# Performance work log

Hardware: AMD Instinct MI355X
Metric: run time of the kernel (lower is better)

The kernel has to match this reference:

```python
import jax, jax.numpy as jnp
import numpy as np

N = 100000
E = 1600000
H = 8
C = 16
DIM = 128
EDGE_DIM = 32


def setup_inputs() -> dict:
    key = jax.random.key(0)
    ks = jax.random.split(key, 7)
    s = 1.0 / np.sqrt(DIM)
    return {
        "x": jax.random.normal(ks[0], (N, DIM), dtype=jnp.float32),
        "edge_index": jax.random.randint(ks[1], (2, E), 0, N, dtype=jnp.int32),
        "edge_attr": jax.random.normal(ks[2], (E, EDGE_DIM), dtype=jnp.float32),
        "Wq": jax.random.normal(ks[3], (H * C, DIM), dtype=jnp.float32) * s,
        "Wk": jax.random.normal(ks[4], (H * C, DIM), dtype=jnp.float32) * s,
        "Wv": jax.random.normal(ks[5], (H * C, DIM), dtype=jnp.float32) * s,
        "We": jax.random.normal(ks[6], (H, EDGE_DIM), dtype=jnp.float32) * (1.0 / np.sqrt(EDGE_DIM)),
    }


def reference(x, edge_index, edge_attr, Wq, Wk, Wv, We):
    # Node projections: [N, H, C]
    q = (x @ Wq.T).reshape(N, H, C)
    k = (x @ Wk.T).reshape(N, H, C)
    v = (x @ Wv.T).reshape(N, H, C)

    src, dst = edge_index[0], edge_index[1]

    # Per-edge attention logits with edge bias: [E, H]
    edge_bias = edge_attr @ We.T
    scores = jnp.einsum("ehc,ehc->eh", q[dst], k[src]) / np.sqrt(C) + edge_bias

    # Numerically-stable segment softmax over destination groups
    seg_max = jax.ops.segment_max(scores, dst, num_segments=N)  # [N, H]
    ex = jnp.exp(scores - seg_max[dst])
    denom = jax.ops.segment_sum(ex, dst, num_segments=N)  # [N, H]
    alpha = ex / denom[dst]  # [E, H]

    # Scale gathered values and scatter-add to destinations
    msgs = v[src] * alpha[:, :, None]  # [E, H, C]
    out = jax.ops.segment_sum(msgs, dst, num_segments=N)  # [N, H, C]
    return out.reshape(N, H * C)
```

## Files before the change

### kernel.cpp

```cpp
#include <hip/hip_runtime.h>


typedef unsigned int uint32;

__device__ inline unsigned short f2bf(float f) {
    uint32 u = __float_as_uint(f);
    uint32 r = u + 0x7fffu + ((u >> 16) & 1u);
    return (unsigned short)(r >> 16);
}

template <int CTRL>
__device__ inline float dpp_mov(float v) {
    return __int_as_float(__builtin_amdgcn_update_dpp(
        0, __float_as_int(v), CTRL, 0xF, 0xF, true));
}

__global__ __launch_bounds__(256) void qkv_count_kernel(
    const float* __restrict__ x,
    const float* __restrict__ Wq,
    const float* __restrict__ Wk,
    const float* __restrict__ Wv,
    const float* __restrict__ We,
    const float* __restrict__ edge_attr,
    const int* __restrict__ edge_index,
    float* __restrict__ q,
    unsigned short* __restrict__ kbf,
    unsigned short* __restrict__ vbf,
    float* __restrict__ ebias,
    int* __restrict__ counts,
    int N, int E)
{
    if (blockIdx.y == 6) {
        int idx = blockIdx.x * 256 + threadIdx.x;
        if (idx * 4 + 3 < E) {
            int4 d4 = ((const int4*)(edge_index + E))[idx];
            atomicAdd(&counts[d4.x], 1);
            atomicAdd(&counts[d4.y], 1);
            atomicAdd(&counts[d4.z], 1);
            atomicAdd(&counts[d4.w], 1);
        } else {
            for (int e = idx * 4; e < E; ++e)
                atomicAdd(&counts[edge_index[(size_t)E + e]], 1);
        }
        return;
    }

    if (blockIdx.y == 7) {
        const int t  = threadIdx.x;
        const int h  = t & 7;
        const int er = t >> 3;
        float4 wreg[8];
#pragma unroll
        for (int i = 0; i < 8; ++i)
            wreg[i] = *(const float4*)(We + h * 32 + i * 4);
        const int e0 = blockIdx.x * 1024;
        for (int it = 0; it < 32; ++it) {
            int e = e0 + it * 32 + er;
            if (e < E) {
                const float* ea = edge_attr + (size_t)e * 32;
                float s = 0.f;
#pragma unroll
                for (int i = 0; i < 8; ++i) {
                    float4 a = *(const float4*)(ea + i * 4);
                    float4 w = wreg[i];
                    s += a.x * w.x + a.y * w.y + a.z * w.z + a.w * w.w;
                }
                ebias[(size_t)e * 8 + h] = s;
            }
        }
        return;
    }

    const int nb = blockIdx.x * 64;
    const int cb = blockIdx.y * 64;
    const float* __restrict__ W = (cb < 128) ? Wq : (cb < 256) ? Wk : Wv;
    const int wrow0 = cb & 127;

    __shared__ float As[16][68];
    __shared__ float Bs[16][68];

    const int tid = threadIdx.x;
    const int tx = tid & 15;
    const int ty = tid >> 4;

    float acc[4][4] = {};

    const int lrow = tid >> 2;
    const int lk   = (tid & 3) * 4;
    const int n_load = nb + lrow;

    for (int k0 = 0; k0 < 128; k0 += 16) {
        float4 a = make_float4(0.f, 0.f, 0.f, 0.f);
        if (n_load < N)
            a = *(const float4*)(x + (size_t)n_load * 128 + k0 + lk);
        float4 b = *(const float4*)(W + (size_t)(wrow0 + lrow) * 128 + k0 + lk);
        As[lk + 0][lrow] = a.x; As[lk + 1][lrow] = a.y;
        As[lk + 2][lrow] = a.z; As[lk + 3][lrow] = a.w;
        Bs[lk + 0][lrow] = b.x; Bs[lk + 1][lrow] = b.y;
        Bs[lk + 2][lrow] = b.z; Bs[lk + 3][lrow] = b.w;
        __syncthreads();
#pragma unroll
        for (int kk = 0; kk < 16; ++kk) {
            float4 av = *(const float4*)&As[kk][ty * 4];
            float4 bv = *(const float4*)&Bs[kk][tx * 4];
            float avr[4] = {av.x, av.y, av.z, av.w};
            float bvr[4] = {bv.x, bv.y, bv.z, bv.w};
#pragma unroll
            for (int i = 0; i < 4; ++i)
#pragma unroll
                for (int j = 0; j < 4; ++j)
                    acc[i][j] = fmaf(avr[i], bvr[j], acc[i][j]);
        }
        __syncthreads();
    }

#pragma unroll
    for (int i = 0; i < 4; ++i) {
        int n = nb + ty * 4 + i;
        if (n >= N) continue;
        if (cb < 128) {
            float4 o = make_float4(acc[i][0], acc[i][1], acc[i][2], acc[i][3]);
            *(float4*)(q + (size_t)n * 128 + wrow0 + tx * 4) = o;
        } else {
            unsigned short* kv = (cb < 256) ? kbf : vbf;
            ushort4 o;
            o.x = f2bf(acc[i][0]); o.y = f2bf(acc[i][1]);
            o.z = f2bf(acc[i][2]); o.w = f2bf(acc[i][3]);
            *(ushort4*)(kv + (size_t)n * 128 + wrow0 + tx * 4) = o;
        }
    }
}

__global__ __launch_bounds__(256) void scan_pass1(
    const int* __restrict__ counts, int* __restrict__ blocksums, int N)
{
    __shared__ int red[256];
    int base = blockIdx.x * 512;
    int t = threadIdx.x;
    int s = 0;
    if (base + t < N)       s += counts[base + t];
    if (base + 256 + t < N) s += counts[base + 256 + t];
    red[t] = s;
    __syncthreads();
    for (int off = 128; off > 0; off >>= 1) {
        if (t < off) red[t] += red[t + off];
        __syncthreads();
    }
    if (t == 0) blocksums[blockIdx.x] = red[0];
}

__global__ __launch_bounds__(256) void scan_pass2(
    const int* __restrict__ blocksums, int* __restrict__ blockbase, int NB)
{
    __shared__ int sc[256];
    int t = threadIdx.x;
    int v = (t < NB) ? blocksums[t] : 0;
    sc[t] = v;
    __syncthreads();
    for (int off = 1; off < 256; off <<= 1) {
        int tmp = (t >= off) ? sc[t - off] : 0;
        __syncthreads();
        sc[t] += tmp;
        __syncthreads();
    }
    if (t < NB) blockbase[t] = sc[t] - v;
}

__global__ __launch_bounds__(256) void scan_pass3(
    const int* __restrict__ counts, const int* __restrict__ blockbase,
    int* __restrict__ offsets, int* __restrict__ cursor, int N)
{
    __shared__ int sc[256];
    int base = blockIdx.x * 512;
    int t = threadIdx.x;
    int i0 = base + 2 * t, i1 = i0 + 1;
    int c0 = (i0 < N) ? counts[i0] : 0;
    int c1 = (i1 < N) ? counts[i1] : 0;
    int pair = c0 + c1;
    sc[t] = pair;
    __syncthreads();
    for (int off = 1; off < 256; off <<= 1) {
        int tmp = (t >= off) ? sc[t - off] : 0;
        __syncthreads();
        sc[t] += tmp;
        __syncthreads();
    }
    int ex = sc[t] - pair + blockbase[blockIdx.x];
    if (i0 < N) { offsets[i0] = ex;      cursor[i0] = ex; }
    if (i1 < N) { offsets[i1] = ex + c0; cursor[i1] = ex + c0; }
}

__global__ __launch_bounds__(256) void scatter_kernel(
    const int* __restrict__ edge_index,
    int* __restrict__ cursor,
    int2* __restrict__ perm,
    int E)
{
    int e = blockIdx.x * 256 + threadIdx.x;
    if (e >= E) return;
    int s = edge_index[e];
    int d = edge_index[(size_t)E + e];
    int pos = atomicAdd(&cursor[d], 1);
    perm[pos] = make_int2(s, e);
}

template <bool USE_BIAS>
__global__ __launch_bounds__(256) void attn_fused_kernel(
    const float* __restrict__ q,
    const unsigned short* __restrict__ kbf,
    const unsigned short* __restrict__ vbf,
    const float* __restrict__ ebias,
    const float* __restrict__ edge_attr,
    const float* __restrict__ We,
    const int* __restrict__ offsets,
    const int* __restrict__ counts,
    const int2* __restrict__ perm,
    float* __restrict__ out,
    int N)
{
    const int d    = blockIdx.x * 4 + (threadIdx.x >> 6);
    const int lane = threadIdx.x & 63;
    if (d >= N) return;
    const int h = lane >> 3;
    const int j = lane & 7;

    float4 we4 = make_float4(0.f, 0.f, 0.f, 0.f);
    if (!USE_BIAS) we4 = *(const float4*)(We + h * 32 + j * 4);

    const float2 q2 = *(const float2*)(q + (size_t)d * 128 + lane * 2);
    const float qx = q2.x * 0.25f;
    const float qy = q2.y * 0.25f;

    const int start = offsets[d];
    const int cnt   = counts[d];

    float denom = 0.f, accx = 0.f, accy = 0.f;

    for (int i0 = 0; i0 < cnt; i0 += 64) {
        int m = min(64, cnt - i0);
        int2 pv = make_int2(0, 0);
        if (lane < m) pv = perm[start + i0 + lane];

        int src = __shfl(pv.x, 0), e = __shfl(pv.y, 0);
        uint32 kk2 = *(const uint32*)(kbf + (size_t)src * 128 + lane * 2);
        uint32 vv2 = *(const uint32*)(vbf + (size_t)src * 128 + lane * 2);
        float bias = 0.f;
        float4 ea  = make_float4(0.f, 0.f, 0.f, 0.f);
        if (USE_BIAS) bias = ebias[(size_t)e * 8 + h];
        else          ea   = *(const float4*)(edge_attr + (size_t)e * 32 + j * 4);

        for (int t = 0; t < m; ++t) {
            uint32 ck = kk2, cv = vv2;
            float cb = bias;
            float4 cea = ea;
            if (t + 1 < m) {
                int ns = __shfl(pv.x, t + 1), ne = __shfl(pv.y, t + 1);
                kk2 = *(const uint32*)(kbf + (size_t)ns * 128 + lane * 2);
                vv2 = *(const uint32*)(vbf + (size_t)ns * 128 + lane * 2);
                if (USE_BIAS) bias = ebias[(size_t)ne * 8 + h];
                else          ea   = *(const float4*)(edge_attr + (size_t)ne * 32 + j * 4);
            }
            float kx = __uint_as_float(ck << 16);
            float ky = __uint_as_float(ck & 0xffff0000u);
            float part = qx * kx + qy * ky;
            if (!USE_BIAS)
                part += cea.x * we4.x + cea.y * we4.y
                      + cea.z * we4.z + cea.w * we4.w;
            part += dpp_mov<0xB1>(part);
            part += dpp_mov<0x4E>(part);
            part += dpp_mov<0x141>(part);
            float ev = __expf(USE_BIAS ? part + cb : part);
            denom += ev;
            float vx = __uint_as_float(cv << 16);
            float vy = __uint_as_float(cv & 0xffff0000u);
            accx = fmaf(ev, vx, accx);
            accy = fmaf(ev, vy, accy);
        }
    }

    float inv = denom > 0.f ? 1.f / denom : 0.f;
    *(float2*)(out + (size_t)d * 128 + lane * 2) = make_float2(accx * inv, accy * inv);
}

extern "C" void kernel_launch(void* const* d_in, const int* in_sizes, int n_in,
                              void* d_out, int out_size, void* d_ws, size_t ws_size,
                              hipStream_t stream) {
    const float* x          = (const float*)d_in[0];
    const int*   edge_index = (const int*)d_in[1];
    const float* edge_attr  = (const float*)d_in[2];
    const float* Wq         = (const float*)d_in[3];
    const float* Wk         = (const float*)d_in[4];
    const float* Wv         = (const float*)d_in[5];
    const float* We         = (const float*)d_in[6];
    float* out = (float*)d_out;

    const int N = in_sizes[0] / 128;
    const int E = in_sizes[1] / 2;

    float* q = (float*)d_ws;
    unsigned short* kbf = (unsigned short*)(q + (size_t)N * 128);
    unsigned short* vbf = kbf + (size_t)N * 128;
    int2* perm = (int2*)(vbf + (size_t)N * 128);
    int* counts    = (int*)(perm + E);
    int* offsets   = counts + N;
    int* cursor    = offsets + N;
    int* blocksums = cursor + N;
    int* blockbase = blocksums + 256;
    float* ebias   = (float*)(blockbase + 256);

    const size_t need_bias =
        (size_t)((char*)(ebias + (size_t)E * 8) - (char*)d_ws);
    const bool use_bias = ws_size >= need_bias;

    hipMemsetAsync(counts, 0, (size_t)N * sizeof(int), stream);

    const int nxb = (N + 63) / 64;
    dim3 g1(nxb, use_bias ? 8 : 7);
    qkv_count_kernel<<<g1, 256, 0, stream>>>(x, Wq, Wk, Wv, We, edge_attr,
                                             edge_index, q, kbf, vbf, ebias,
                                             counts, N, E);

    const int NB = (N + 511) / 512;
    scan_pass1<<<NB, 256, 0, stream>>>(counts, blocksums, N);
    scan_pass2<<<1, 256, 0, stream>>>(blocksums, blockbase, NB);
    scan_pass3<<<NB, 256, 0, stream>>>(counts, blockbase, offsets, cursor, N);

    scatter_kernel<<<(E + 255) / 256, 256, 0, stream>>>(edge_index, cursor,
                                                        perm, E);

    if (use_bias)
        attn_fused_kernel<true><<<(N + 3) / 4, 256, 0, stream>>>(
            q, kbf, vbf, ebias, edge_attr, We, offsets, counts, perm, out, N);
    else
        attn_fused_kernel<false><<<(N + 3) / 4, 256, 0, stream>>>(
            q, kbf, vbf, ebias, edge_attr, We, offsets, counts, perm, out, N);
}
```

Before: 829.8 us.

## Interleave K/V bf16, fuse edge-bias into scatter in CSR order, reuse x tile

The edge-bias computation moves from the projection kernel into the scatter kernel. Each bias row is written at its destination-sorted position, so the attention kernel reads biases contiguously instead of by random edge id. K and V are packed into one interleaved bf16 buffer, so each source gather is a single 8-byte load. The projection kernel now keeps the whole x tile in shared memory and loops over all six weight chunks with a double-buffered weight tile, so x is read once instead of six times. In exchange, the larger shared-memory footprint lowers occupancy, and the scatter kernel does more per-thread work and register pressure.

```diff
diff --git a/kernel.cpp b/kernel.cpp
--- a/kernel.cpp
+++ b/kernel.cpp
@@ -7,6 +7,10 @@
     uint32 u = __float_as_uint(f);
     uint32 r = u + 0x7fffu + ((u >> 16) & 1u);
     return (unsigned short)(r >> 16);
+}
+
+__device__ inline uint32 pack2bf(float a, float b) {
+    return (uint32)f2bf(a) | ((uint32)f2bf(b) << 16);
 }
 
 template <int CTRL>
@@ -20,17 +24,13 @@
     const float* __restrict__ Wq,
     const float* __restrict__ Wk,
     const float* __restrict__ Wv,
-    const float* __restrict__ We,
-    const float* __restrict__ edge_attr,
     const int* __restrict__ edge_index,
     float* __restrict__ q,
-    unsigned short* __restrict__ kbf,
-    unsigned short* __restrict__ vbf,
-    float* __restrict__ ebias,
+    uint32* __restrict__ kvb,
     int* __restrict__ counts,
     int N, int E)
 {
-    if (blockIdx.y == 6) {
+    if (blockIdx.y == 1) {
         int idx = blockIdx.x * 256 + threadIdx.x;
         if (idx * 4 + 3 < E) {
             int4 d4 = ((const int4*)(edge_index + E))[idx];
@@ -39,94 +39,91 @@
             atomicAdd(&counts[d4.z], 1);
             atomicAdd(&counts[d4.w], 1);
         } else {
-            for (int e = idx * 4; e < E; ++e)
+            for (int e = idx * 4; e < E && e >= 0; ++e)
                 atomicAdd(&counts[edge_index[(size_t)E + e]], 1);
         }
         return;
     }
 
-    if (blockIdx.y == 7) {
-        const int t  = threadIdx.x;
-        const int h  = t & 7;
-        const int er = t >> 3;
-        float4 wreg[8];
-#pragma unroll
-        for (int i = 0; i < 8; ++i)
-            wreg[i] = *(const float4*)(We + h * 32 + i * 4);
-        const int e0 = blockIdx.x * 1024;
-        for (int it = 0; it < 32; ++it) {
-            int e = e0 + it * 32 + er;
-            if (e < E) {
-                const float* ea = edge_attr + (size_t)e * 32;
-                float s = 0.f;
-#pragma unroll
-                for (int i = 0; i < 8; ++i) {
-                    float4 a = *(const float4*)(ea + i * 4);
-                    float4 w = wreg[i];
-                    s += a.x * w.x + a.y * w.y + a.z * w.z + a.w * w.w;
-                }
-                ebias[(size_t)e * 8 + h] = s;
-            }
-        }
-        return;
-    }
-
     const int nb = blockIdx.x * 64;
-    const int cb = blockIdx.y * 64;
-    const float* __restrict__ W = (cb < 128) ? Wq : (cb < 256) ? Wk : Wv;
-    const int wrow0 = cb & 127;
-
-    __shared__ float As[16][68];
-    __shared__ float Bs[16][68];
+    if (nb >= N) return;
+
+    __shared__ float As[128][68];
+    __shared__ float Bs[2][16][68];
 
     const int tid = threadIdx.x;
     const int tx = tid & 15;
     const int ty = tid >> 4;
-
-    float acc[4][4] = {};
-
     const int lrow = tid >> 2;
     const int lk   = (tid & 3) * 4;
     const int n_load = nb + lrow;
 
+#pragma unroll
     for (int k0 = 0; k0 < 128; k0 += 16) {
         float4 a = make_float4(0.f, 0.f, 0.f, 0.f);
         if (n_load < N)
             a = *(const float4*)(x + (size_t)n_load * 128 + k0 + lk);
-        float4 b = *(const float4*)(W + (size_t)(wrow0 + lrow) * 128 + k0 + lk);
-        As[lk + 0][lrow] = a.x; As[lk + 1][lrow] = a.y;
-        As[lk + 2][lrow] = a.z; As[lk + 3][lrow] = a.w;
-        Bs[lk + 0][lrow] = b.x; Bs[lk + 1][lrow] = b.y;
-        Bs[lk + 2][lrow] = b.z; Bs[lk + 3][lrow] = b.w;
-        __syncthreads();
-#pragma unroll
-        for (int kk = 0; kk < 16; ++kk) {
-            float4 av = *(const float4*)&As[kk][ty * 4];
-            float4 bv = *(const float4*)&Bs[kk][tx * 4];
-            float avr[4] = {av.x, av.y, av.z, av.w};
-            float bvr[4] = {bv.x, bv.y, bv.z, bv.w};
-#pragma unroll
-            for (int i = 0; i < 4; ++i)
-#pragma unroll
-                for (int j = 0; j < 4; ++j)
-                    acc[i][j] = fmaf(avr[i], bvr[j], acc[i][j]);
-        }
-        __syncthreads();
-    }
-
-#pragma unroll
-    for (int i = 0; i < 4; ++i) {
-        int n = nb + ty * 4 + i;
-        if (n >= N) continue;
-        if (cb < 128) {
-            float4 o = make_float4(acc[i][0], acc[i][1], acc[i][2], acc[i][3]);
-            *(float4*)(q + (size_t)n * 128 + wrow0 + tx * 4) = o;
-        } else {
-            unsigned short* kv = (cb < 256) ? kbf : vbf;
-            ushort4 o;
-            o.x = f2bf(acc[i][0]); o.y = f2bf(acc[i][1]);
-            o.z = f2bf(acc[i][2]); o.w = f2bf(acc[i][3]);
-            *(ushort4*)(kv + (size_t)n * 128 + wrow0 + tx * 4) = o;
+        As[k0 + lk + 0][lrow] = a.x; As[k0 + lk + 1][lrow] = a.y;
+        As[k0 + lk + 2][lrow] = a.z; As[k0 + lk + 3][lrow] = a.w;
+    }
+    {
+        float4 b = *(const float4*)(Wq + (size_t)lrow * 128 + lk);
+        Bs[0][lk + 0][lrow] = b.x; Bs[0][lk + 1][lrow] = b.y;
+        Bs[0][lk + 2][lrow] = b.z; Bs[0][lk + 3][lrow] = b.w;
+    }
+    __syncthreads();
+
+#pragma unroll 1
+    for (int chunk = 0; chunk < 6; ++chunk) {
+        float acc[4][4] = {};
+#pragma unroll 2
+        for (int k0i = 0; k0i < 8; ++k0i) {
+            const int buf = k0i & 1;
+            const int idx = chunk * 8 + k0i + 1;
+            if (idx < 48) {
+                const int nc  = idx >> 3;
+                const int nk0 = (idx & 7) * 16;
+                const float* __restrict__ W =
+                    (nc < 2) ? Wq : (nc < 4) ? Wk : Wv;
+                const int wr0 = (nc & 1) * 64;
+                float4 b = *(const float4*)(W + (size_t)(wr0 + lrow) * 128
+                                            + nk0 + lk);
+                Bs[buf ^ 1][lk + 0][lrow] = b.x;
+                Bs[buf ^ 1][lk + 1][lrow] = b.y;
+                Bs[buf ^ 1][lk + 2][lrow] = b.z;
+                Bs[buf ^ 1][lk + 3][lrow] = b.w;
+            }
+#pragma unroll
+            for (int kk = 0; kk < 16; ++kk) {
+                float4 av = *(const float4*)&As[k0i * 16 + kk][ty * 4];
+                float4 bv = *(const float4*)&Bs[buf][kk][tx * 4];
+                float avr[4] = {av.x, av.y, av.z, av.w};
+                float bvr[4] = {bv.x, bv.y, bv.z, bv.w};
+#pragma unroll
+                for (int i = 0; i < 4; ++i)
+#pragma unroll
+                    for (int j = 0; j < 4; ++j)
+                        acc[i][j] = fmaf(avr[i], bvr[j], acc[i][j]);
+            }
+            __syncthreads();
+        }
+
+        const int wrow0 = (chunk & 1) * 64;
+#pragma unroll
+        for (int i = 0; i < 4; ++i) {
+            int n = nb + ty * 4 + i;
+            if (n >= N) continue;
+            if (chunk < 2) {
+                float4 o = make_float4(acc[i][0], acc[i][1],
+                                       acc[i][2], acc[i][3]);
+                *(float4*)(q + (size_t)n * 128 + wrow0 + tx * 4) = o;
+            } else {
+                const int ch0 = wrow0 + tx * 4;
+                uint32* rp = kvb + (size_t)n * 128 + ch0
+                           + ((chunk >= 4) ? 1 : 0);
+                rp[0] = pack2bf(acc[i][0], acc[i][1]);
+                rp[2] = pack2bf(acc[i][2], acc[i][3]);
+            }
         }
     }
 }
@@ -190,26 +187,54 @@
     if (i1 < N) { offsets[i1] = ex + c0; cursor[i1] = ex + c0; }
 }
 
+template <bool WITH_BIAS>
 __global__ __launch_bounds__(256) void scatter_kernel(
     const int* __restrict__ edge_index,
+    const float* __restrict__ edge_attr,
+    const float* __restrict__ We,
     int* __restrict__ cursor,
     int2* __restrict__ perm,
+    float* __restrict__ pbias,
     int E)
 {
     int e = blockIdx.x * 256 + threadIdx.x;
     if (e >= E) return;
     int s = edge_index[e];
     int d = edge_index[(size_t)E + e];
+
+    float b[8];
+    if (WITH_BIAS) {
+        const float* ea = edge_attr + (size_t)e * 32;
+        float4 a[8];
+#pragma unroll
+        for (int i = 0; i < 8; ++i) a[i] = *(const float4*)(ea + i * 4);
+#pragma unroll
+        for (int h = 0; h < 8; ++h) {
+            float sum = 0.f;
+#pragma unroll
+            for (int i = 0; i < 8; ++i) {
+                float4 w = *(const float4*)(We + h * 32 + i * 4);
+                sum += a[i].x * w.x + a[i].y * w.y
+                     + a[i].z * w.z + a[i].w * w.w;
+            }
+            b[h] = sum;
+        }
+    }
+
     int pos = atomicAdd(&cursor[d], 1);
     perm[pos] = make_int2(s, e);
+    if (WITH_BIAS) {
+        float* pb = pbias + (size_t)pos * 8;
+        *(float4*)(pb + 0) = make_float4(b[0], b[1], b[2], b[3]);
+        *(float4*)(pb + 4) = make_float4(b[4], b[5], b[6], b[7]);
+    }
 }
 
 template <bool USE_BIAS>
 __global__ __launch_bounds__(256) void attn_fused_kernel(
     const float* __restrict__ q,
-    const unsigned short* __restrict__ kbf,
-    const unsigned short* __restrict__ vbf,
-    const float* __restrict__ ebias,
+    const uint32* __restrict__ kvb,
+    const float* __restrict__ pbias,
     const float* __restrict__ edge_attr,
     const float* __restrict__ We,
     const int* __restrict__ offsets,
@@ -242,26 +267,28 @@
         if (lane < m) pv = perm[start + i0 + lane];
 
         int src = __shfl(pv.x, 0), e = __shfl(pv.y, 0);
-        uint32 kk2 = *(const uint32*)(kbf + (size_t)src * 128 + lane * 2);
-        uint32 vv2 = *(const uint32*)(vbf + (size_t)src * 128 + lane * 2);
+        uint2 kv = *(const uint2*)(kvb + (size_t)src * 128 + lane * 2);
         float bias = 0.f;
         float4 ea  = make_float4(0.f, 0.f, 0.f, 0.f);
-        if (USE_BIAS) bias = ebias[(size_t)e * 8 + h];
+        if (USE_BIAS) bias = pbias[(size_t)(start + i0) * 8 + h];
         else          ea   = *(const float4*)(edge_attr + (size_t)e * 32 + j * 4);
 
         for (int t = 0; t < m; ++t) {
-            uint32 ck = kk2, cv = vv2;
-            float cb = bias;
+            uint2 ckv = kv;
+            float cb  = bias;
             float4 cea = ea;
             if (t + 1 < m) {
-                int ns = __shfl(pv.x, t + 1), ne = __shfl(pv.y, t + 1);
-                kk2 = *(const uint32*)(kbf + (size_t)ns * 128 + lane * 2);
-                vv2 = *(const uint32*)(vbf + (size_t)ns * 128 + lane * 2);
-                if (USE_BIAS) bias = ebias[(size_t)ne * 8 + h];
-                else          ea   = *(const float4*)(edge_attr + (size_t)ne * 32 + j * 4);
-            }
-            float kx = __uint_as_float(ck << 16);
-            float ky = __uint_as_float(ck & 0xffff0000u);
+                int ns = __shfl(pv.x, t + 1);
+                kv = *(const uint2*)(kvb + (size_t)ns * 128 + lane * 2);
+                if (USE_BIAS) {
+                    bias = pbias[(size_t)(start + i0 + t + 1) * 8 + h];
+                } else {
+                    int ne = __shfl(pv.y, t + 1);
+                    ea = *(const float4*)(edge_attr + (size_t)ne * 32 + j * 4);
+                }
+            }
+            float kx = __uint_as_float(ckv.x << 16);
+            float ky = __uint_as_float(ckv.x & 0xffff0000u);
             float part = qx * kx + qy * ky;
             if (!USE_BIAS)
                 part += cea.x * we4.x + cea.y * we4.y
@@ -269,12 +296,10 @@
             part += dpp_mov<0xB1>(part);
             part += dpp_mov<0x4E>(part);
             part += dpp_mov<0x141>(part);
-            float ev = __expf(USE_BIAS ? part + cb : part);
+            float ev = __expf(part + cb);
             denom += ev;
-            float vx = __uint_as_float(cv << 16);
-            float vy = __uint_as_float(cv & 0xffff0000u);
-            accx = fmaf(ev, vx, accx);
-            accy = fmaf(ev, vy, accy);
+            accx = fmaf(ev, __uint_as_float(ckv.y << 16), accx);
+            accy = fmaf(ev, __uint_as_float(ckv.y & 0xffff0000u), accy);
         }
     }
 
@@ -298,40 +323,44 @@
     const int E = in_sizes[1] / 2;
 
     float* q = (float*)d_ws;
-    unsigned short* kbf = (unsigned short*)(q + (size_t)N * 128);
-    unsigned short* vbf = kbf + (size_t)N * 128;
-    int2* perm = (int2*)(vbf + (size_t)N * 128);
+    uint32* kvb = (uint32*)(q + (size_t)N * 128);
+    int2* perm = (int2*)(kvb + (size_t)N * 128);
     int* counts    = (int*)(perm + E);
     int* offsets   = counts + N;
     int* cursor    = offsets + N;
     int* blocksums = cursor + N;
     int* blockbase = blocksums + 256;
-    float* ebias   = (float*)(blockbase + 256);
+    float* pbias   = (float*)(blockbase + 256);
 
     const size_t need_bias =
-        (size_t)((char*)(ebias + (size_t)E * 8) - (char*)d_ws);
+        (size_t)((char*)(pbias + (size_t)E * 8) - (char*)d_ws);
     const bool use_bias = ws_size >= need_bias;
 
     hipMemsetAsync(counts, 0, (size_t)N * sizeof(int), stream);
 
-    const int nxb = (N + 63) / 64;
-    dim3 g1(nxb, use_bias ? 8 : 7);
-    qkv_count_kernel<<<g1, 256, 0, stream>>>(x, Wq, Wk, Wv, We, edge_attr,
-                                             edge_index, q, kbf, vbf, ebias,
-                                             counts, N, E);
+    const int nxb_g = (N + 63) / 64;
+    const int nxb_h = (E + 1023) / 1024;
+    const int nxb = nxb_g > nxb_h ? nxb_g : nxb_h;
+    dim3 g1(nxb, 2);
+    qkv_count_kernel<<<g1, 256, 0, stream>>>(x, Wq, Wk, Wv, edge_index,
+                                             q, kvb, counts, N, E);
 
     const int NB = (N + 511) / 512;
     scan_pass1<<<NB, 256, 0, stream>>>(counts, blocksums, N);
     scan_pass2<<<1, 256, 0, stream>>>(blocksums, blockbase, NB);
     scan_pass3<<<NB, 256, 0, stream>>>(counts, blockbase, offsets, cursor, N);
 
-    scatter_kernel<<<(E + 255) / 256, 256, 0, stream>>>(edge_index, cursor,
-                                                        perm, E);
+    if (use_bias)
+        scatter_kernel<true><<<(E + 255) / 256, 256, 0, stream>>>(
+            edge_index, edge_attr, We, cursor, perm, pbias, E);
+    else
+        scatter_kernel<false><<<(E + 255) / 256, 256, 0, stream>>>(
+            edge_index, edge_attr, We, cursor, perm, pbias, E);
 
     if (use_bias)
         attn_fused_kernel<true><<<(N + 3) / 4, 256, 0, stream>>>(
-            q, kbf, vbf, ebias, edge_attr, We, offsets, counts, perm, out, N);
+            q, kvb, pbias, edge_attr, We, offsets, counts, perm, out, N);
     else
         attn_fused_kernel<false><<<(N + 3) / 4, 256, 0, stream>>>(
-            q, kbf, vbf, ebias, edge_attr, We, offsets, counts, perm, out, N);
-}
+            q, kvb, pbias, edge_attr, We, offsets, counts, perm, out, N);
+}
```

After: 764.6 us. 1.09x faster.
